# Optimization experiments

Measured on AMD Instinct MI355X. Metric: run time of the kernel, lower is better.

The kernel has to match this reference:

```python
import jax, jax.numpy as jnp
import numpy as np

B_GRAPHS, NODES, K, NGRID, C, BASIS = 8, 256, 16, 12, 128, 128
M = B_GRAPHS * NODES
TWO_PI = 2.0 * np.pi


def _knn_edges(pos):
    # within-graph kNN (includes self, like torch_cluster.knn(x, x, k))
    p = pos.reshape(B_GRAPHS, NODES, 3)
    d2 = jnp.sum((p[:, :, None, :] - p[:, None, :, :]) ** 2, axis=-1)  # [B,n,n]
    _, idx = jax.lax.top_k(-d2, K)                                     # [B,n,K]
    offs = jnp.arange(B_GRAPHS)[:, None, None] * NODES
    src = (idx + offs).reshape(-1)                                     # neighbor j (edge_index[0] after flip)
    tgt = jnp.broadcast_to(jnp.arange(NODES)[None, :, None] + offs, idx.shape).reshape(-1)
    return src, tgt


def _rff(x, B):
    proj = TWO_PI * (x @ B)
    return jnp.concatenate([jnp.cos(proj), jnp.sin(proj)], axis=-1)


def _basis_mlp(a, B, W1, b1, W2, b2):
    h = jax.nn.gelu(_rff(a, B) @ W1 + b1)
    return jax.nn.gelu(h @ W2 + b2)


def _layernorm(x, g, b):
    mu = jnp.mean(x, axis=-1, keepdims=True)
    var = jnp.var(x, axis=-1, keepdims=True)
    return (x - mu) * jax.lax.rsqrt(var + 1e-5) * g + b


def _interaction(x, kb_x, kb_R, src, tgt, Wkx, WkR, g, b, W1, b1, W2, b2, s):
    # spatial depthwise conv: gather -> per-edge kernel * x_j -> scatter-mean
    msg = (kb_x @ Wkx) * x[src]                                   # [E,NGRID,C]
    x1 = jax.ops.segment_sum(msg, tgt, num_segments=M) / K        # mean aggr (every node has exactly K in-edges)
    # fiber (orientation) depthwise conv
    kR = kb_R @ WkR                                               # [NGRID,NGRID,C]
    x2 = jnp.einsum('moc,poc->mpc', x1, kR) / NGRID
    # ConvNeXt-style pointwise MLP with layer scale + residual
    h = _layernorm(x2, g, b)
    h = jax.nn.gelu(h @ W1 + b1) @ W2 + b2
    return x + s * h


def _forward(x, pos_Rd, grid, Bx, BR, Wx1, bx1, Wx2, bx2, WR1, bR1, WR2, bR2,
             l1_Wkx, l1_WkR, l1_g, l1_b, l1_W1, l1_b1, l1_W2, l1_b2, l1_s,
             l2_Wkx, l2_WkR, l2_g, l2_b, l2_W1, l2_b1, l2_W2, l2_b2, l2_s):
    src, tgt = _knn_edges(pos_Rd)
    # equivariant edge attributes (edge_attr_r3s2_grid_mode)
    rel_pos_R = jnp.einsum('mi,ni->mn', grid, grid)[:, :, None]            # [NGRID,NGRID,1]
    rel_pos = pos_Rd[src] - pos_Rd[tgt]                                    # [E,3]
    rel_pos_z = jnp.einsum('ei,ni->en', rel_pos, grid)                     # [E,NGRID]
    rel_pos_xy = jnp.linalg.norm(rel_pos[:, None, :] - rel_pos_z[:, :, None] * grid[None, :, :], axis=-1)
    rel_pos_x = jnp.stack([rel_pos_xy, rel_pos_z], axis=-1)                # [E,NGRID,2]
    kb_x = _basis_mlp(rel_pos_x, Bx, Wx1, bx1, Wx2, bx2)                   # [E,NGRID,BASIS]
    kb_R = _basis_mlp(rel_pos_R, BR, WR1, bR1, WR2, bR2)                   # [NGRID,NGRID,BASIS]
    x = _interaction(x, kb_x, kb_R, src, tgt, l1_Wkx, l1_WkR, l1_g, l1_b, l1_W1, l1_b1, l1_W2, l1_b2, l1_s)
    x = _interaction(x, kb_x, kb_R, src, tgt, l2_Wkx, l2_WkR, l2_g, l2_b, l2_W1, l2_b1, l2_W2, l2_b2, l2_s)
    return x


def setup_inputs() -> dict:
    key = jax.random.key(0)
    ks = jax.random.split(key, 20)
    nrm = lambda k, shape, s: jax.random.normal(k, shape, jnp.float32) * s
    inp = {}
    inp['x'] = nrm(ks[0], (M, NGRID, C), 1.0)
    inp['pos_Rd'] = nrm(ks[1], (M, 3), 1.0)
    g = jax.random.normal(ks[2], (NGRID, 3), jnp.float32)
    inp['grid'] = g / jnp.linalg.norm(g, axis=-1, keepdims=True)           # unit S2 grid
    inp['Bx'] = nrm(ks[3], (2, C // 2), 10.0)                              # RFF, sigma=[10,10]
    inp['BR'] = nrm(ks[4], (1, C // 2), 10.0)                              # RFF, sigma=[10]
    inp['Wx1'] = nrm(ks[5], (C, C), C ** -0.5); inp['bx1'] = jnp.zeros((C,))
    inp['Wx2'] = nrm(ks[6], (C, BASIS), C ** -0.5); inp['bx2'] = jnp.zeros((BASIS,))
    inp['WR1'] = nrm(ks[7], (C, C), C ** -0.5); inp['bR1'] = jnp.zeros((C,))
    inp['WR2'] = nrm(ks[8], (C, BASIS), C ** -0.5); inp['bR2'] = jnp.zeros((BASIS,))
    i = 9
    for l in ('l1', 'l2'):
        inp[l + '_Wkx'] = nrm(ks[i], (BASIS, C), BASIS ** -0.5); i += 1
        inp[l + '_WkR'] = nrm(ks[i], (BASIS, C), BASIS ** -0.5); i += 1
        inp[l + '_g'] = jnp.ones((C,)); inp[l + '_b'] = jnp.zeros((C,))
        inp[l + '_W1'] = nrm(ks[i], (C, 4 * C), C ** -0.5); i += 1
        inp[l + '_b1'] = jnp.zeros((4 * C,))
        inp[l + '_W2'] = nrm(ks[i], (4 * C, C), (4 * C) ** -0.5); i += 1
        inp[l + '_b2'] = jnp.zeros((C,))
        inp[l + '_s'] = jnp.full((C,), 1e-2)
    return inp


def reference(x, pos_Rd, grid, Bx, BR, Wx1, bx1, Wx2, bx2, WR1, bR1, WR2, bR2,
              l1_Wkx, l1_WkR, l1_g, l1_b, l1_W1, l1_b1, l1_W2, l1_b2, l1_s,
              l2_Wkx, l2_WkR, l2_g, l2_b, l2_W1, l2_b1, l2_W2, l2_b2, l2_s):
    return _forward(x, pos_Rd, grid, Bx, BR, Wx1, bx1, Wx2, bx2, WR1, bR1, WR2, bR2,
                    l1_Wkx, l1_WkR, l1_g, l1_b, l1_W1, l1_b1, l1_W2, l1_b2, l1_s,
                    l2_Wkx, l2_WkR, l2_g, l2_b, l2_W1, l2_b1, l2_W2, l2_b2, l2_s)
```

## Files before the change

### kernel.cpp

```cpp
#include <hip/hip_runtime.h>
#include <hip/hip_bf16.h>
#include <math.h>

#define BG 8
#define NNODES 256
#define KNN 16
#define NG 12
#define CH 128
#define MTOT 2048
#define TWO_PI_F 6.283185307179586f

typedef __attribute__((ext_vector_type(8))) short bfrag;
typedef __attribute__((ext_vector_type(4))) float f32x4;


__device__ __forceinline__ float gelu_t(float x) {
  float x3 = x * x * x;
  float y = 0.7978845608028654f * (x + 0.044715f * x3);
  float e = __expf(2.0f * y);
  float th = 1.0f - 2.0f / (e + 1.0f);
  return 0.5f * x * (1.0f + th);
}

__device__ __forceinline__ unsigned packbf2(float a, float b) {
  unsigned ua = __float_as_uint(a), ub = __float_as_uint(b);
  ua = (ua + 0x7fffu + ((ua >> 16) & 1u)) >> 16;
  ub = (ub + 0x7fffu + ((ub >> 16) & 1u)) >> 16;
  return ua | (ub << 16);
}
__device__ __forceinline__ unsigned short f2bf(float f) {
  unsigned u = __float_as_uint(f);
  u = (u + 0x7fffu + ((u >> 16) & 1u)) >> 16;
  return (unsigned short)u;
}
__device__ __forceinline__ float ubf_lo(unsigned p) { return __uint_as_float(p << 16); }
__device__ __forceinline__ float ubf_hi(unsigned p) { return __uint_as_float(p & 0xffff0000u); }

__device__ __forceinline__ float gelu_s(float x) {
  const float A  = -2.0f * 0.7978845608028654f * 1.4426950408889634f;
  const float CA = A * 0.044715f;
  float x2 = x * x;
  float q  = __builtin_fmaf(CA, x2, A);
  float t  = x * q;
  float e; asm("v_exp_f32 %0, %1" : "=v"(e) : "v"(t));
  float d = 1.0f + e;
  float r; asm("v_rcp_f32 %0, %1" : "=v"(r) : "v"(d));
  return x * r;
}

__device__ __forceinline__ unsigned pkcvt(float a, float b) {
  unsigned r;
  asm("v_cvt_pk_bf16_f32 %0, %1, %2" : "=v"(r) : "v"(a), "v"(b));
  return r;
}

__device__ __forceinline__ void cossin(float w, float& c, float& s) {
  float f; asm("v_fract_f32 %0, %1" : "=v"(f) : "v"(w));
  asm("v_cos_f32 %0, %1" : "=v"(c) : "v"(f));
  asm("v_sin_f32 %0, %1" : "=v"(s) : "v"(f));
}

__device__ __forceinline__ unsigned long long shfl_xor64(unsigned long long v, int st) {
  unsigned lo = (unsigned)v, hi = (unsigned)(v >> 32);
  lo = __shfl_xor(lo, st, 64);
  hi = __shfl_xor(hi, st, 64);
  return ((unsigned long long)hi << 32) | lo;
}


__global__ __launch_bounds__(256) void knn_kernel(const float* __restrict__ pos,
                                                  int* __restrict__ knn) {
  __shared__ float sx[NNODES], sy[NNODES], sz[NNODES];
  int w = threadIdx.x >> 6, lane = threadIdx.x & 63;
  int node = blockIdx.x * 4 + w;
  int b = node >> 8;
  int gbase = b * NNODES;
  int t = threadIdx.x;
  sx[t] = pos[(gbase + t) * 3 + 0];
  sy[t] = pos[(gbase + t) * 3 + 1];
  sz[t] = pos[(gbase + t) * 3 + 2];
  __syncthreads();
  int i = node & 255;
  float xi = sx[i], yi = sy[i], zi = sz[i];
  unsigned long long key[4];
#pragma unroll
  for (int u = 0; u < 4; ++u) {
    int j = lane * 4 + u;
    float dx = xi - sx[j], dy = yi - sy[j], dz = zi - sz[j];
    float d = dx * dx + dy * dy + dz * dz;
    key[u] = ((unsigned long long)__float_as_uint(d) << 32) | (unsigned)j;
  }
  {
    unsigned long long tmp;
#define CSWAP(a, bq) if (key[bq] < key[a]) { tmp = key[a]; key[a] = key[bq]; key[bq] = tmp; }
    CSWAP(0, 1) CSWAP(2, 3) CSWAP(0, 2) CSWAP(1, 3) CSWAP(1, 2)
#undef CSWAP
  }
  int ptr = 0;
#pragma unroll 1
  for (int r = 0; r < KNN; ++r) {
    unsigned long long cand = (ptr < 4) ? key[ptr] : ~0ULL;
    unsigned long long mn = cand;
#pragma unroll
    for (int st = 1; st < 64; st <<= 1) {
      unsigned long long o = shfl_xor64(mn, st);
      if (o < mn) mn = o;
    }
    if (cand == mn) ptr++;
    if (lane == 0) knn[node * KNN + r] = gbase + (int)(mn & 0xffffffffu);
  }
}


__global__ void kbr_kernel(const float* __restrict__ grid, const float* __restrict__ BR,
                           const float* __restrict__ WR1, const float* __restrict__ bR1,
                           const float* __restrict__ WR2, const float* __restrict__ bR2,
                           const float* __restrict__ WkR1, const float* __restrict__ WkR2,
                           float* __restrict__ kR1, float* __restrict__ kR2) {
  int r = blockIdx.x;
  int p = r / NG, o = r % NG;
  int c = threadIdx.x;
  float a = grid[p * 3 + 0] * grid[o * 3 + 0] + grid[p * 3 + 1] * grid[o * 3 + 1] +
            grid[p * 3 + 2] * grid[o * 3 + 2];
  __shared__ float fb[CH], hh[CH];
  {
    int j = c & 63;
    float pv = TWO_PI_F * (a * BR[j]);
    fb[c] = (c < 64) ? cosf(pv) : sinf(pv);
  }
  __syncthreads();
  float acc = bR1[c];
  for (int i = 0; i < CH; ++i) acc += fb[i] * WR1[i * CH + c];
  float h1 = gelu_t(acc);
  __syncthreads();
  hh[c] = h1;
  __syncthreads();
  acc = bR2[c];
  for (int i = 0; i < CH; ++i) acc += hh[i] * WR2[i * CH + c];
  float h2 = gelu_t(acc);
  __syncthreads();
  fb[c] = h2;
  __syncthreads();
  float t1 = 0.f, t2 = 0.f;
  for (int i = 0; i < CH; ++i) {
    float v = fb[i];
    t1 += v * WkR1[i * CH + c];
    t2 += v * WkR2[i * CH + c];
  }
  kR1[r * CH + c] = t1;
  kR2[r * CH + c] = t2;
}


__global__ void einsum_kernel(const float* __restrict__ x1, const float* __restrict__ kR,
                              float* __restrict__ x2) {
  int m = blockIdx.x, c = threadIdx.x;
  float v[NG];
#pragma unroll
  for (int o = 0; o < NG; ++o) v[o] = x1[((size_t)m * NG + o) * CH + c];
#pragma unroll
  for (int p = 0; p < NG; ++p) {
    float acc = 0.f;
#pragma unroll
    for (int o = 0; o < NG; ++o) acc += v[o] * kR[(p * NG + o) * CH + c];
    x2[((size_t)m * NG + p) * CH + c] = acc * (1.0f / NG);
  }
}


__device__ __forceinline__ void pack_body(const float* __restrict__ W, int K, int N,
                                          unsigned short* __restrict__ out, int tid) {
  int lane = tid & 63;
  int t = tid >> 6;
  int ksteps = K / 32;
  int ks = t % ksteps, tile = t / ksteps;
  int col = tile * 16 + (lane & 15);
  int k0 = ks * 32 + (lane >> 4) * 8;
#pragma unroll
  for (int j = 0; j < 8; ++j)
    out[(size_t)tid * 8 + j] = f2bf(W[(size_t)(k0 + j) * N + col]);
}

__global__ __launch_bounds__(256) void pack_all_kernel(
    const float* __restrict__ W1a, const float* __restrict__ W2a,
    const float* __restrict__ W1b, const float* __restrict__ W2b,
    const float* __restrict__ wx1, const float* __restrict__ wx2,
    const float* __restrict__ wk1, const float* __restrict__ wk2,
    unsigned short* __restrict__ o1a, unsigned short* __restrict__ o2a,
    unsigned short* __restrict__ o1b, unsigned short* __restrict__ o2b,
    unsigned short* __restrict__ ox1, unsigned short* __restrict__ ox2,
    unsigned short* __restrict__ ok1, unsigned short* __restrict__ ok2) {
  int blk = blockIdx.x;
  if (blk < 32)        pack_body(W1a, CH, 4 * CH, o1a, blk * 256 + threadIdx.x);
  else if (blk < 64)   pack_body(W2a, 4 * CH, CH, o2a, (blk - 32) * 256 + threadIdx.x);
  else if (blk < 96)   pack_body(W1b, CH, 4 * CH, o1b, (blk - 64) * 256 + threadIdx.x);
  else if (blk < 128)  pack_body(W2b, 4 * CH, CH, o2b, (blk - 96) * 256 + threadIdx.x);
  else if (blk < 136)  pack_body(wx1, CH, CH, ox1, (blk - 128) * 256 + threadIdx.x);
  else if (blk < 144)  pack_body(wx2, CH, CH, ox2, (blk - 136) * 256 + threadIdx.x);
  else if (blk < 152)  pack_body(wk1, CH, CH, ok1, (blk - 144) * 256 + threadIdx.x);
  else                 pack_body(wk2, CH, CH, ok2, (blk - 152) * 256 + threadIdx.x);
}


__global__ __launch_bounds__(256) void kbx_fused_kernel(
    const float* __restrict__ pos, const int* __restrict__ knn,
    const float* __restrict__ grid, const float* __restrict__ Bx,
    const uint4* __restrict__ w1f, const float* __restrict__ bx1,
    const uint4* __restrict__ w2f, const float* __restrict__ bx2,
    const uint4* __restrict__ wk1f, const uint4* __restrict__ wk2f,
    const float* __restrict__ x, const float* __restrict__ kR,
    uint2* __restrict__ t2g, float* __restrict__ x2out) {
  __shared__ uint4 hb[4][3][256];
  float* x1s = (float*)hb;
  int m = blockIdx.x;
  int tid = threadIdx.x, lane = tid & 63, w = tid >> 6;
  int r = lane & 15, gq = lane >> 4;

  int src = knn[m * KNN + r];
  float rx = pos[src * 3 + 0] - pos[m * 3 + 0];
  float ry = pos[src * 3 + 1] - pos[m * 3 + 1];
  float rz = pos[src * 3 + 2] - pos[m * 3 + 2];

  float4 brA0 = *(const float4*)(Bx + gq * 8);
  float4 brA1 = *(const float4*)(Bx + gq * 8 + 4);
  float4 brB0 = *(const float4*)(Bx + 32 + gq * 8);
  float4 brB1 = *(const float4*)(Bx + 32 + gq * 8 + 4);
  float4 bzA0 = *(const float4*)(Bx + 64 + gq * 8);
  float4 bzA1 = *(const float4*)(Bx + 64 + gq * 8 + 4);
  float4 bzB0 = *(const float4*)(Bx + 96 + gq * 8);
  float4 bzB1 = *(const float4*)(Bx + 96 + gq * 8 + 4);
  float brA[8] = {brA0.x, brA0.y, brA0.z, brA0.w, brA1.x, brA1.y, brA1.z, brA1.w};
  float brB[8] = {brB0.x, brB0.y, brB0.z, brB0.w, brB1.x, brB1.y, brB1.z, brB1.w};
  float bzA[8] = {bzA0.x, bzA0.y, bzA0.z, bzA0.w, bzA1.x, bzA1.y, bzA1.z, bzA1.w};
  float bzB[8] = {bzB0.x, bzB0.y, bzB0.z, bzB0.w, bzB1.x, bzB1.y, bzB1.z, bzB1.w};

  bfrag ff[3][4];
#pragma unroll
  for (int t = 0; t < 3; ++t) {
    int o = w * 3 + t;
    float gx = grid[o * 3 + 0], gy = grid[o * 3 + 1], gz = grid[o * 3 + 2];
    float z = rx * gx + ry * gy + rz * gz;
    float ux = rx - z * gx, uy = ry - z * gy, uz = rz - z * gz;
    float rxy = sqrtf(ux * ux + uy * uy + uz * uz);
    float cA[8], sA[8], cB[8], sB[8];
#pragma unroll
    for (int u = 0; u < 8; ++u) {
      float wA = __builtin_fmaf(z, bzA[u], rxy * brA[u]);
      float wB = __builtin_fmaf(z, bzB[u], rxy * brB[u]);
      cossin(wA, cA[u], sA[u]);
      cossin(wB, cB[u], sB[u]);
    }
    uint4 q;
    q.x = pkcvt(cA[0], cA[1]); q.y = pkcvt(cA[2], cA[3]);
    q.z = pkcvt(cA[4], cA[5]); q.w = pkcvt(cA[6], cA[7]);
    ff[t][0] = __builtin_bit_cast(bfrag, q);
    q.x = pkcvt(cB[0], cB[1]); q.y = pkcvt(cB[2], cB[3]);
    q.z = pkcvt(cB[4], cB[5]); q.w = pkcvt(cB[6], cB[7]);
    ff[t][1] = __builtin_bit_cast(bfrag, q);
    q.x = pkcvt(sA[0], sA[1]); q.y = pkcvt(sA[2], sA[3]);
    q.z = pkcvt(sA[4], sA[5]); q.w = pkcvt(sA[6], sA[7]);
    ff[t][2] = __builtin_bit_cast(bfrag, q);
    q.x = pkcvt(sB[0], sB[1]); q.y = pkcvt(sB[2], sB[3]);
    q.z = pkcvt(sB[4], sB[5]); q.w = pkcvt(sB[6], sB[7]);
    ff[t][3] = __builtin_bit_cast(bfrag, q);
  }

#pragma unroll 1
  for (int jt = 0; jt < 8; ++jt) {
    bfrag wf[4];
#pragma unroll
    for (int ks = 0; ks < 4; ++ks)
      wf[ks] = __builtin_bit_cast(bfrag, w1f[(jt * 4 + ks) * 64 + lane]);
    float4 bb = *(const float4*)(bx1 + jt * 16 + gq * 4);
    int cu = jt * 2 + (gq >> 1);
#pragma unroll
    for (int t = 0; t < 3; ++t) {
      f32x4 acc;
      acc[0] = bb.x; acc[1] = bb.y; acc[2] = bb.z; acc[3] = bb.w;
#pragma unroll
      for (int ks = 0; ks < 4; ++ks)
        acc = __builtin_amdgcn_mfma_f32_16x16x32_bf16(wf[ks], ff[t][ks], acc, 0, 0, 0);
      unsigned p0 = pkcvt(gelu_s(acc[0]), gelu_s(acc[1]));
      unsigned p1 = pkcvt(gelu_s(acc[2]), gelu_s(acc[3]));
      ((uint2*)&hb[w][t][0])[r * 32 + ((cu ^ r) << 1) + (gq & 1)] = make_uint2(p0, p1);
    }
  }
  bfrag h1f[3][4];
#pragma unroll
  for (int t = 0; t < 3; ++t)
#pragma unroll
    for (int ks = 0; ks < 4; ++ks)
      h1f[t][ks] = __builtin_bit_cast(bfrag, hb[w][t][r * 16 + ((ks * 4 + gq) ^ r)]);

#pragma unroll 1
  for (int jt = 0; jt < 8; ++jt) {
    bfrag wf[4];
#pragma unroll
    for (int ks = 0; ks < 4; ++ks)
      wf[ks] = __builtin_bit_cast(bfrag, w2f[(jt * 4 + ks) * 64 + lane]);
    float4 bb = *(const float4*)(bx2 + jt * 16 + gq * 4);
    int cu = jt * 2 + (gq >> 1);
#pragma unroll
    for (int t = 0; t < 3; ++t) {
      f32x4 acc;
      acc[0] = bb.x; acc[1] = bb.y; acc[2] = bb.z; acc[3] = bb.w;
#pragma unroll
      for (int ks = 0; ks < 4; ++ks)
        acc = __builtin_amdgcn_mfma_f32_16x16x32_bf16(wf[ks], h1f[t][ks], acc, 0, 0, 0);
      unsigned p0 = pkcvt(gelu_s(acc[0]), gelu_s(acc[1]));
      unsigned p1 = pkcvt(gelu_s(acc[2]), gelu_s(acc[3]));
      ((uint2*)&hb[w][t][0])[r * 32 + ((cu ^ r) << 1) + (gq & 1)] = make_uint2(p0, p1);
    }
  }
  bfrag h2f[3][4];
#pragma unroll
  for (int t = 0; t < 3; ++t)
#pragma unroll
    for (int ks = 0; ks < 4; ++ks)
      h2f[t][ks] = __builtin_bit_cast(bfrag, hb[w][t][r * 16 + ((ks * 4 + gq) ^ r)]);

  __syncthreads();

#pragma unroll 1
  for (int jt = 0; jt < 8; ++jt) {
    bfrag wf[4];
#pragma unroll
    for (int ks = 0; ks < 4; ++ks)
      wf[ks] = __builtin_bit_cast(bfrag, wk1f[(jt * 4 + ks) * 64 + lane]);
#pragma unroll
    for (int t = 0; t < 3; ++t) {
      int o = w * 3 + t;
      f32x4 acc;
      acc[0] = 0.f; acc[1] = 0.f; acc[2] = 0.f; acc[3] = 0.f;
#pragma unroll
      for (int ks = 0; ks < 4; ++ks)
        acc = __builtin_amdgcn_mfma_f32_16x16x32_bf16(wf[ks], h2f[t][ks], acc, 0, 0, 0);
      float4 xv = *(const float4*)(x + ((size_t)src * NG + o) * CH + jt * 16 + gq * 4);
      acc[0] *= xv.x; acc[1] *= xv.y; acc[2] *= xv.z; acc[3] *= xv.w;
#pragma unroll
      for (int st = 1; st < 16; st <<= 1) {
        acc[0] += __shfl_xor(acc[0], st, 64);
        acc[1] += __shfl_xor(acc[1], st, 64);
        acc[2] += __shfl_xor(acc[2], st, 64);
        acc[3] += __shfl_xor(acc[3], st, 64);
      }
      if (r == 0) {
        int c0 = jt * 16 + gq * 4;
        float4 sv;
        sv.x = acc[0] * (1.f / 16.f); sv.y = acc[1] * (1.f / 16.f);
        sv.z = acc[2] * (1.f / 16.f); sv.w = acc[3] * (1.f / 16.f);
        *(float4*)&x1s[o * CH + c0] = sv;
      }
    }
  }

#pragma unroll 1
  for (int jt = 0; jt < 8; ++jt) {
    bfrag wf[4];
#pragma unroll
    for (int ks = 0; ks < 4; ++ks)
      wf[ks] = __builtin_bit_cast(bfrag, wk2f[(jt * 4 + ks) * 64 + lane]);
#pragma unroll
    for (int t = 0; t < 3; ++t) {
      int tile = m * NG + w * 3 + t;
      f32x4 acc;
      acc[0] = 0.f; acc[1] = 0.f; acc[2] = 0.f; acc[3] = 0.f;
#pragma unroll
      for (int ks = 0; ks < 4; ++ks)
        acc = __builtin_amdgcn_mfma_f32_16x16x32_bf16(wf[ks], h2f[t][ks], acc, 0, 0, 0);
      uint2 pv;
      pv.x = pkcvt(acc[0], acc[1]);
      pv.y = pkcvt(acc[2], acc[3]);
      t2g[((size_t)tile * 8 + jt) * 64 + lane] = pv;
    }
  }
  __syncthreads();

  int c = tid & 127, p0 = tid >> 7;
  float v[NG];
#pragma unroll
  for (int o = 0; o < NG; ++o) v[o] = x1s[o * CH + c];
#pragma unroll
  for (int pp = 0; pp < 6; ++pp) {
    int p = p0 * 6 + pp;
    float acc = 0.f;
#pragma unroll
    for (int o = 0; o < NG; ++o) acc += v[o] * kR[(p * NG + o) * CH + c];
    x2out[((size_t)m * NG + p) * CH + c] = acc * (1.0f / NG);
  }
}


__global__ __launch_bounds__(256) void msg3b_kernel(
    const float* __restrict__ x, const int* __restrict__ knn,
    const uint2* __restrict__ t2g, const float* __restrict__ kR,
    float* __restrict__ x2out) {
  __shared__ float x1s[NG][CH];
  int m = blockIdx.x;
  int tid = threadIdx.x, lane = tid & 63, w = tid >> 6;
  int r = lane & 15, gq = lane >> 4;
  int src = knn[m * KNN + r];

#pragma unroll 1
  for (int jt = 0; jt < 8; ++jt) {
#pragma unroll
    for (int t = 0; t < 3; ++t) {
      int o = w * 3 + t;
      int tile = m * NG + o;
      uint2 tv = t2g[((size_t)tile * 8 + jt) * 64 + lane];
      float4 xv = *(const float4*)(x + ((size_t)src * NG + o) * CH + jt * 16 + gq * 4);
      float a0 = ubf_lo(tv.x) * xv.x;
      float a1 = ubf_hi(tv.x) * xv.y;
      float a2 = ubf_lo(tv.y) * xv.z;
      float a3 = ubf_hi(tv.y) * xv.w;
#pragma unroll
      for (int st = 1; st < 16; st <<= 1) {
        a0 += __shfl_xor(a0, st, 64);
        a1 += __shfl_xor(a1, st, 64);
        a2 += __shfl_xor(a2, st, 64);
        a3 += __shfl_xor(a3, st, 64);
      }
      if (r == 0) {
        int c0 = jt * 16 + gq * 4;
        x1s[o][c0 + 0] = a0 * (1.f / 16.f);
        x1s[o][c0 + 1] = a1 * (1.f / 16.f);
        x1s[o][c0 + 2] = a2 * (1.f / 16.f);
        x1s[o][c0 + 3] = a3 * (1.f / 16.f);
      }
    }
  }
  __syncthreads();

  int c = tid & 127, p0 = tid >> 7;
  float v[NG];
#pragma unroll
  for (int o = 0; o < NG; ++o) v[o] = x1s[o][c];
#pragma unroll
  for (int pp = 0; pp < 6; ++pp) {
    int p = p0 * 6 + pp;
    float acc = 0.f;
#pragma unroll
    for (int o = 0; o < NG; ++o) acc += v[o] * kR[(p * NG + o) * CH + c];
    x2out[((size_t)m * NG + p) * CH + c] = acc * (1.0f / NG);
  }
}


__global__ __launch_bounds__(256) void msg_mfma_kernel(
    const float* __restrict__ x, const float* __restrict__ pos,
    const int* __restrict__ knn, const float* __restrict__ grid,
    const float* __restrict__ Bx,
    const uint4* __restrict__ w1f, const float* __restrict__ bx1,
    const uint4* __restrict__ w2f, const float* __restrict__ bx2,
    const uint4* __restrict__ wkf,
    float* __restrict__ x1out) {
  __shared__ uint4 hb[4][3][256];
  int m = blockIdx.x;
  int tid = threadIdx.x, lane = tid & 63, w = tid >> 6;
  int r = lane & 15, gq = lane >> 4;

  int src = knn[m * KNN + r];
  float rx = pos[src * 3 + 0] - pos[m * 3 + 0];
  float ry = pos[src * 3 + 1] - pos[m * 3 + 1];
  float rz = pos[src * 3 + 2] - pos[m * 3 + 2];

  bfrag ff[3][4];
#pragma unroll
  for (int t = 0; t < 3; ++t) {
    int o = w * 3 + t;
    float gx = grid[o * 3 + 0], gy = grid[o * 3 + 1], gz = grid[o * 3 + 2];
    float z = rx * gx + ry * gy + rz * gz;
    float ux = rx - z * gx, uy = ry - z * gy, uz = rz - z * gz;
    float rxy = sqrtf(ux * ux + uy * uy + uz * uz);
#pragma unroll
    for (int ks = 0; ks < 4; ++ks) {
      uint4 q;
      unsigned pk[4];
#pragma unroll
      for (int jh = 0; jh < 4; ++jh) {
        float v[2];
#pragma unroll
        for (int u = 0; u < 2; ++u) {
          int i = ks * 32 + gq * 8 + jh * 2 + u;
          int j = i & 63;
          float pv = TWO_PI_F * (rxy * Bx[j] + z * Bx[64 + j]);
          v[u] = (i < 64) ? __cosf(pv) : __sinf(pv);
        }
        pk[jh] = packbf2(v[0], v[1]);
      }
      q.x = pk[0]; q.y = pk[1]; q.z = pk[2]; q.w = pk[3];
      ff[t][ks] = __builtin_bit_cast(bfrag, q);
    }
  }

#pragma unroll 1
  for (int jt = 0; jt < 8; ++jt) {
    bfrag wf[4];
#pragma unroll
    for (int ks = 0; ks < 4; ++ks)
      wf[ks] = __builtin_bit_cast(bfrag, w1f[(jt * 4 + ks) * 64 + lane]);
    float4 bb = *(const float4*)(bx1 + jt * 16 + gq * 4);
    int cu = jt * 2 + (gq >> 1);
#pragma unroll
    for (int t = 0; t < 3; ++t) {
      f32x4 acc;
      acc[0] = bb.x; acc[1] = bb.y; acc[2] = bb.z; acc[3] = bb.w;
#pragma unroll
      for (int ks = 0; ks < 4; ++ks)
        acc = __builtin_amdgcn_mfma_f32_16x16x32_bf16(wf[ks], ff[t][ks], acc, 0, 0, 0);
      unsigned p0 = packbf2(gelu_t(acc[0]), gelu_t(acc[1]));
      unsigned p1 = packbf2(gelu_t(acc[2]), gelu_t(acc[3]));
      ((uint2*)&hb[w][t][0])[r * 32 + ((cu ^ r) << 1) + (gq & 1)] = make_uint2(p0, p1);
    }
  }
  bfrag h1f[3][4];
#pragma unroll
  for (int t = 0; t < 3; ++t)
#pragma unroll
    for (int ks = 0; ks < 4; ++ks)
      h1f[t][ks] = __builtin_bit_cast(bfrag, hb[w][t][r * 16 + ((ks * 4 + gq) ^ r)]);

#pragma unroll 1
  for (int jt = 0; jt < 8; ++jt) {
    bfrag wf[4];
#pragma unroll
    for (int ks = 0; ks < 4; ++ks)
      wf[ks] = __builtin_bit_cast(bfrag, w2f[(jt * 4 + ks) * 64 + lane]);
    float4 bb = *(const float4*)(bx2 + jt * 16 + gq * 4);
    int cu = jt * 2 + (gq >> 1);
#pragma unroll
    for (int t = 0; t < 3; ++t) {
      f32x4 acc;
      acc[0] = bb.x; acc[1] = bb.y; acc[2] = bb.z; acc[3] = bb.w;
#pragma unroll
      for (int ks = 0; ks < 4; ++ks)
        acc = __builtin_amdgcn_mfma_f32_16x16x32_bf16(wf[ks], h1f[t][ks], acc, 0, 0, 0);
      unsigned p0 = packbf2(gelu_t(acc[0]), gelu_t(acc[1]));
      unsigned p1 = packbf2(gelu_t(acc[2]), gelu_t(acc[3]));
      ((uint2*)&hb[w][t][0])[r * 32 + ((cu ^ r) << 1) + (gq & 1)] = make_uint2(p0, p1);
    }
  }
  bfrag h2f[3][4];
#pragma unroll
  for (int t = 0; t < 3; ++t)
#pragma unroll
    for (int ks = 0; ks < 4; ++ks)
      h2f[t][ks] = __builtin_bit_cast(bfrag, hb[w][t][r * 16 + ((ks * 4 + gq) ^ r)]);

#pragma unroll 1
  for (int jt = 0; jt < 8; ++jt) {
    bfrag wf[4];
#pragma unroll
    for (int ks = 0; ks < 4; ++ks)
      wf[ks] = __builtin_bit_cast(bfrag, wkf[(jt * 4 + ks) * 64 + lane]);
#pragma unroll
    for (int t = 0; t < 3; ++t) {
      int o = w * 3 + t;
      f32x4 acc;
      acc[0] = 0.f; acc[1] = 0.f; acc[2] = 0.f; acc[3] = 0.f;
#pragma unroll
      for (int ks = 0; ks < 4; ++ks)
        acc = __builtin_amdgcn_mfma_f32_16x16x32_bf16(wf[ks], h2f[t][ks], acc, 0, 0, 0);
      float4 xv = *(const float4*)(x + ((size_t)src * NG + o) * CH + jt * 16 + gq * 4);
      acc[0] *= xv.x; acc[1] *= xv.y; acc[2] *= xv.z; acc[3] *= xv.w;
#pragma unroll
      for (int st = 1; st < 16; st <<= 1) {
        acc[0] += __shfl_xor(acc[0], st, 64);
        acc[1] += __shfl_xor(acc[1], st, 64);
        acc[2] += __shfl_xor(acc[2], st, 64);
        acc[3] += __shfl_xor(acc[3], st, 64);
      }
      if (r == 0) {
        float4 sv;
        sv.x = acc[0] * (1.f / 16.f); sv.y = acc[1] * (1.f / 16.f);
        sv.z = acc[2] * (1.f / 16.f); sv.w = acc[3] * (1.f / 16.f);
        *(float4*)(x1out + ((size_t)m * NG + o) * CH + jt * 16 + gq * 4) = sv;
      }
    }
  }
}


__global__ __launch_bounds__(256) void mlp_mfma_kernel(
    const float* __restrict__ xin, const float* __restrict__ x2,
    const float* __restrict__ g, const float* __restrict__ b,
    const uint4* __restrict__ w1t, const float* __restrict__ b1,
    const uint4* __restrict__ w2t, const float* __restrict__ b2,
    const float* __restrict__ s, float* __restrict__ xout) {
  __shared__ uint4 smem[1280];
  int tid = threadIdx.x;
  int rowbase = blockIdx.x * 16;

  {
    int row = tid >> 4, p = tid & 15;
    const float4* xr = (const float4*)(x2 + (size_t)(rowbase + row) * CH + p * 8);
    float4 v0 = xr[0], v1 = xr[1];
    float sum = v0.x + v0.y + v0.z + v0.w + v1.x + v1.y + v1.z + v1.w;
    sum += __shfl_xor(sum, 1, 64); sum += __shfl_xor(sum, 2, 64);
    sum += __shfl_xor(sum, 4, 64); sum += __shfl_xor(sum, 8, 64);
    float mu = sum * (1.0f / CH);
    float sq = 0.f;
    {
      float d;
      d = v0.x - mu; sq += d * d; d = v0.y - mu; sq += d * d;
      d = v0.z - mu; sq += d * d; d = v0.w - mu; sq += d * d;
      d = v1.x - mu; sq += d * d; d = v1.y - mu; sq += d * d;
      d = v1.z - mu; sq += d * d; d = v1.w - mu; sq += d * d;
    }
    sq += __shfl_xor(sq, 1, 64); sq += __shfl_xor(sq, 2, 64);
    sq += __shfl_xor(sq, 4, 64); sq += __shfl_xor(sq, 8, 64);
    float rstd = rsqrtf(sq * (1.0f / CH) + 1e-5f);
    const float4* gv = (const float4*)(g + p * 8);
    const float4* bv = (const float4*)(b + p * 8);
    float4 g0 = gv[0], g1 = gv[1], b0 = bv[0], b1v = bv[1];
    float n0 = (v0.x - mu) * rstd * g0.x + b0.x;
    float n1 = (v0.y - mu) * rstd * g0.y + b0.y;
    float n2 = (v0.z - mu) * rstd * g0.z + b0.z;
    float n3 = (v0.w - mu) * rstd * g0.w + b0.w;
    float n4 = (v1.x - mu) * rstd * g1.x + b1v.x;
    float n5 = (v1.y - mu) * rstd * g1.y + b1v.y;
    float n6 = (v1.z - mu) * rstd * g1.z + b1v.z;
    float n7 = (v1.w - mu) * rstd * g1.w + b1v.w;
    uint4 pk;
    pk.x = packbf2(n0, n1); pk.y = packbf2(n2, n3);
    pk.z = packbf2(n4, n5); pk.w = packbf2(n6, n7);
    smem[row * 16 + (p ^ row)] = pk;
  }
  __syncthreads();

  int lane = tid & 63, w = tid >> 6;
  int r = lane & 15, gq = lane >> 4;

  bfrag xf[4];
#pragma unroll
  for (int ks = 0; ks < 4; ++ks) {
    uint4 raw = smem[r * 16 + ((ks * 4 + gq) ^ r)];
    xf[ks] = __builtin_bit_cast(bfrag, raw);
  }

  uint2* hb2 = (uint2*)smem;
#pragma unroll 1
  for (int jj = 0; jj < 8; ++jj) {
    int jt = w * 8 + jj;
    f32x4 acc;
    {
      float4 bb = *(const float4*)(b1 + jt * 16 + gq * 4);
      acc[0] = bb.x; acc[1] = bb.y; acc[2] = bb.z; acc[3] = bb.w;
    }
#pragma unroll
    for (int ks = 0; ks < 4; ++ks) {
      uint4 raw = w1t[(jt * 4 + ks) * 64 + lane];
      bfrag a = __builtin_bit_cast(bfrag, raw);
      acc = __builtin_amdgcn_mfma_f32_16x16x32_bf16(a, xf[ks], acc, 0, 0, 0);
    }
    unsigned p0 = packbf2(gelu_t(acc[0]), gelu_t(acc[1]));
    unsigned p1 = packbf2(gelu_t(acc[2]), gelu_t(acc[3]));
    int sl = (jt * 2 + (gq >> 1)) ^ r;
    hb2[512 + r * 128 + sl * 2 + (gq & 1)] = make_uint2(p0, p1);
  }
  __syncthreads();

#pragma unroll 1
  for (int cc = 0; cc < 2; ++cc) {
    int ct = w * 2 + cc;
    f32x4 acc;
    {
      float4 bb = *(const float4*)(b2 + ct * 16 + gq * 4);
      acc[0] = bb.x; acc[1] = bb.y; acc[2] = bb.z; acc[3] = bb.w;
    }
#pragma unroll
    for (int ks = 0; ks < 16; ++ks) {
      uint4 hraw = smem[256 + r * 64 + ((ks * 4 + gq) ^ r)];
      bfrag hf = __builtin_bit_cast(bfrag, hraw);
      uint4 wraw = w2t[(ct * 16 + ks) * 64 + lane];
      bfrag wf = __builtin_bit_cast(bfrag, wraw);
      acc = __builtin_amdgcn_mfma_f32_16x16x32_bf16(wf, hf, acc, 0, 0, 0);
    }
    int c0 = ct * 16 + gq * 4;
    size_t ro = (size_t)(rowbase + r) * CH + c0;
    float4 xi = *(const float4*)(xin + ro);
    float4 sv = *(const float4*)(s + c0);
    float4 ov;
    ov.x = xi.x + sv.x * acc[0];
    ov.y = xi.y + sv.y * acc[1];
    ov.z = xi.z + sv.z * acc[2];
    ov.w = xi.w + sv.w * acc[3];
    *(float4*)(xout + ro) = ov;
  }
}


extern "C" void kernel_launch(void* const* d_in, const int* in_sizes, int n_in,
                              void* d_out, int out_size, void* d_ws, size_t ws_size,
                              hipStream_t stream) {
  (void)in_sizes; (void)n_in; (void)out_size;
  const float* x    = (const float*)d_in[0];
  const float* pos  = (const float*)d_in[1];
  const float* grid = (const float*)d_in[2];
  const float* Bx   = (const float*)d_in[3];
  float* out = (float*)d_out;

  char* wsb = (char*)d_ws;
  int* knn   = (int*)wsb;
  float* kR1 = (float*)(wsb + 131072);
  float* kR2 = kR1 + NG * NG * CH;
  float* x1  = kR2 + NG * NG * CH;
  float* x2  = x1 + (size_t)MTOT * NG * CH;
  unsigned short* w1ta = (unsigned short*)(x2 + (size_t)MTOT * NG * CH);
  unsigned short* w2ta = w1ta + 65536;
  unsigned short* w1tb = w2ta + 65536;
  unsigned short* w2tb = w1tb + 65536;
  unsigned short* wx1f = w2tb + 65536;
  unsigned short* wx2f = wx1f + 16384;
  unsigned short* wk1f = wx2f + 16384;
  unsigned short* wk2f = wk1f + 16384;
  uint2* t2g = (uint2*)(wk2f + 16384);
  size_t need = (size_t)26099712 + (size_t)MTOT * NG * 4 * 64 * 16;
  bool big_ws = ws_size >= need;

  knn_kernel<<<MTOT / 4, 256, 0, stream>>>(pos, knn);
  kbr_kernel<<<NG * NG, CH, 0, stream>>>(grid, (const float*)d_in[4],
                                         (const float*)d_in[9], (const float*)d_in[10],
                                         (const float*)d_in[11], (const float*)d_in[12],
                                         (const float*)d_in[14], (const float*)d_in[23],
                                         kR1, kR2);
  pack_all_kernel<<<160, 256, 0, stream>>>(
      (const float*)d_in[17], (const float*)d_in[19],
      (const float*)d_in[26], (const float*)d_in[28],
      (const float*)d_in[5], (const float*)d_in[7],
      (const float*)d_in[13], (const float*)d_in[22],
      w1ta, w2ta, w1tb, w2tb, wx1f, wx2f, wk1f, wk2f);

  if (big_ws) {
    kbx_fused_kernel<<<MTOT, 256, 0, stream>>>(pos, knn, grid, Bx,
        (const uint4*)wx1f, (const float*)d_in[6],
        (const uint4*)wx2f, (const float*)d_in[8],
        (const uint4*)wk1f, (const uint4*)wk2f,
        x, kR1, t2g, x2);
    mlp_mfma_kernel<<<(MTOT * NG) / 16, 256, 0, stream>>>(x, x2,
        (const float*)d_in[15], (const float*)d_in[16],
        (const uint4*)w1ta, (const float*)d_in[18],
        (const uint4*)w2ta, (const float*)d_in[20],
        (const float*)d_in[21], out);
    msg3b_kernel<<<MTOT, 256, 0, stream>>>(out, knn, (const uint2*)t2g, kR2, x2);
    mlp_mfma_kernel<<<(MTOT * NG) / 16, 256, 0, stream>>>(out, x2,
        (const float*)d_in[24], (const float*)d_in[25],
        (const uint4*)w1tb, (const float*)d_in[27],
        (const uint4*)w2tb, (const float*)d_in[29],
        (const float*)d_in[30], out);
  } else {
    msg_mfma_kernel<<<MTOT, 256, 0, stream>>>(x, pos, knn, grid, Bx,
        (const uint4*)wx1f, (const float*)d_in[6],
        (const uint4*)wx2f, (const float*)d_in[8],
        (const uint4*)wk1f, x1);
    einsum_kernel<<<MTOT, CH, 0, stream>>>(x1, kR1, x2);
    mlp_mfma_kernel<<<(MTOT * NG) / 16, 256, 0, stream>>>(x, x2,
        (const float*)d_in[15], (const float*)d_in[16],
        (const uint4*)w1ta, (const float*)d_in[18],
        (const uint4*)w2ta, (const float*)d_in[20],
        (const float*)d_in[21], out);
    msg_mfma_kernel<<<MTOT, 256, 0, stream>>>(out, pos, knn, grid, Bx,
        (const uint4*)wx1f, (const float*)d_in[6],
        (const uint4*)wx2f, (const float*)d_in[8],
        (const uint4*)wk2f, x1);
    einsum_kernel<<<MTOT, CH, 0, stream>>>(x1, kR2, x2);
    mlp_mfma_kernel<<<(MTOT * NG) / 16, 256, 0, stream>>>(out, x2,
        (const float*)d_in[24], (const float*)d_in[25],
        (const uint4*)w1tb, (const float*)d_in[27],
        (const uint4*)w2tb, (const float*)d_in[29],
        (const float*)d_in[30], out);
  }
}
```

Measured before the change: 232.9 us.

## Stream hidden MLP tiles through smaller LDS buffer and raise occupancy bound

The two per-edge basis MLP layers now produce output in chunks of two column tiles, converting each chunk straight into the next layer's k-slice fragment instead of staging the whole hidden layer in LDS. This quarters the shared-memory scratch per block and allows a launch bound of 4 blocks per SM, aiming for higher occupancy. It adds a minimum-occupancy hint that may force register spills, given the large fragment arrays kept in registers.

```diff
diff --git a/kernel.cpp b/kernel.cpp
--- a/kernel.cpp
+++ b/kernel.cpp
@@ -202,7 +202,7 @@
 }
 
 
-__global__ __launch_bounds__(256) void kbx_fused_kernel(
+__global__ __launch_bounds__(256, 4) void kbx_fused_kernel(
     const float* __restrict__ pos, const int* __restrict__ knn,
     const float* __restrict__ grid, const float* __restrict__ Bx,
     const uint4* __restrict__ w1f, const float* __restrict__ bx1,
@@ -210,8 +210,8 @@
     const uint4* __restrict__ wk1f, const uint4* __restrict__ wk2f,
     const float* __restrict__ x, const float* __restrict__ kR,
     uint2* __restrict__ t2g, float* __restrict__ x2out) {
-  __shared__ uint4 hb[4][3][256];
-  float* x1s = (float*)hb;
+  __shared__ uint2 hbuf[4][3][128];
+  float* x1s = (float*)hbuf;
   int m = blockIdx.x;
   int tid = threadIdx.x, lane = tid & 63, w = tid >> 6;
   int r = lane & 15, gq = lane >> 4;
@@ -265,59 +265,63 @@
     ff[t][3] = __builtin_bit_cast(bfrag, q);
   }
 
-#pragma unroll 1
-  for (int jt = 0; jt < 8; ++jt) {
-    bfrag wf[4];
-#pragma unroll
-    for (int ks = 0; ks < 4; ++ks)
-      wf[ks] = __builtin_bit_cast(bfrag, w1f[(jt * 4 + ks) * 64 + lane]);
-    float4 bb = *(const float4*)(bx1 + jt * 16 + gq * 4);
-    int cu = jt * 2 + (gq >> 1);
-#pragma unroll
-    for (int t = 0; t < 3; ++t) {
-      f32x4 acc;
-      acc[0] = bb.x; acc[1] = bb.y; acc[2] = bb.z; acc[3] = bb.w;
-#pragma unroll
-      for (int ks = 0; ks < 4; ++ks)
-        acc = __builtin_amdgcn_mfma_f32_16x16x32_bf16(wf[ks], ff[t][ks], acc, 0, 0, 0);
-      unsigned p0 = pkcvt(gelu_s(acc[0]), gelu_s(acc[1]));
-      unsigned p1 = pkcvt(gelu_s(acc[2]), gelu_s(acc[3]));
-      ((uint2*)&hb[w][t][0])[r * 32 + ((cu ^ r) << 1) + (gq & 1)] = make_uint2(p0, p1);
-    }
-  }
   bfrag h1f[3][4];
-#pragma unroll
-  for (int t = 0; t < 3; ++t)
-#pragma unroll
-    for (int ks = 0; ks < 4; ++ks)
-      h1f[t][ks] = __builtin_bit_cast(bfrag, hb[w][t][r * 16 + ((ks * 4 + gq) ^ r)]);
-
-#pragma unroll 1
-  for (int jt = 0; jt < 8; ++jt) {
-    bfrag wf[4];
-#pragma unroll
-    for (int ks = 0; ks < 4; ++ks)
-      wf[ks] = __builtin_bit_cast(bfrag, w2f[(jt * 4 + ks) * 64 + lane]);
-    float4 bb = *(const float4*)(bx2 + jt * 16 + gq * 4);
-    int cu = jt * 2 + (gq >> 1);
-#pragma unroll
-    for (int t = 0; t < 3; ++t) {
-      f32x4 acc;
-      acc[0] = bb.x; acc[1] = bb.y; acc[2] = bb.z; acc[3] = bb.w;
-#pragma unroll
-      for (int ks = 0; ks < 4; ++ks)
-        acc = __builtin_amdgcn_mfma_f32_16x16x32_bf16(wf[ks], h1f[t][ks], acc, 0, 0, 0);
-      unsigned p0 = pkcvt(gelu_s(acc[0]), gelu_s(acc[1]));
-      unsigned p1 = pkcvt(gelu_s(acc[2]), gelu_s(acc[3]));
-      ((uint2*)&hb[w][t][0])[r * 32 + ((cu ^ r) << 1) + (gq & 1)] = make_uint2(p0, p1);
-    }
-  }
+#pragma unroll 1
+  for (int ks = 0; ks < 4; ++ks) {
+#pragma unroll
+    for (int jq = 0; jq < 2; ++jq) {
+      int jt = ks * 2 + jq;
+      bfrag wf[4];
+#pragma unroll
+      for (int kk = 0; kk < 4; ++kk)
+        wf[kk] = __builtin_bit_cast(bfrag, w1f[(jt * 4 + kk) * 64 + lane]);
+      float4 bb = *(const float4*)(bx1 + jt * 16 + gq * 4);
+#pragma unroll
+      for (int t = 0; t < 3; ++t) {
+        f32x4 acc;
+        acc[0] = bb.x; acc[1] = bb.y; acc[2] = bb.z; acc[3] = bb.w;
+#pragma unroll
+        for (int kk = 0; kk < 4; ++kk)
+          acc = __builtin_amdgcn_mfma_f32_16x16x32_bf16(wf[kk], ff[t][kk], acc, 0, 0, 0);
+        unsigned p0 = pkcvt(gelu_s(acc[0]), gelu_s(acc[1]));
+        unsigned p1 = pkcvt(gelu_s(acc[2]), gelu_s(acc[3]));
+        hbuf[w][t][jq * 64 + r * 4 + gq] = make_uint2(p0, p1);
+      }
+    }
+#pragma unroll
+    for (int t = 0; t < 3; ++t)
+      h1f[t][ks] = __builtin_bit_cast(bfrag,
+          ((const uint4*)&hbuf[w][t][0])[(gq >> 1) * 32 + r * 2 + (gq & 1)]);
+  }
+
   bfrag h2f[3][4];
-#pragma unroll
-  for (int t = 0; t < 3; ++t)
-#pragma unroll
-    for (int ks = 0; ks < 4; ++ks)
-      h2f[t][ks] = __builtin_bit_cast(bfrag, hb[w][t][r * 16 + ((ks * 4 + gq) ^ r)]);
+#pragma unroll 1
+  for (int ks = 0; ks < 4; ++ks) {
+#pragma unroll
+    for (int jq = 0; jq < 2; ++jq) {
+      int jt = ks * 2 + jq;
+      bfrag wf[4];
+#pragma unroll
+      for (int kk = 0; kk < 4; ++kk)
+        wf[kk] = __builtin_bit_cast(bfrag, w2f[(jt * 4 + kk) * 64 + lane]);
+      float4 bb = *(const float4*)(bx2 + jt * 16 + gq * 4);
+#pragma unroll
+      for (int t = 0; t < 3; ++t) {
+        f32x4 acc;
+        acc[0] = bb.x; acc[1] = bb.y; acc[2] = bb.z; acc[3] = bb.w;
+#pragma unroll
+        for (int kk = 0; kk < 4; ++kk)
+          acc = __builtin_amdgcn_mfma_f32_16x16x32_bf16(wf[kk], h1f[t][kk], acc, 0, 0, 0);
+        unsigned p0 = pkcvt(gelu_s(acc[0]), gelu_s(acc[1]));
+        unsigned p1 = pkcvt(gelu_s(acc[2]), gelu_s(acc[3]));
+        hbuf[w][t][jq * 64 + r * 4 + gq] = make_uint2(p0, p1);
+      }
+    }
+#pragma unroll
+    for (int t = 0; t < 3; ++t)
+      h2f[t][ks] = __builtin_bit_cast(bfrag,
+          ((const uint4*)&hbuf[w][t][0])[(gq >> 1) * 32 + r * 2 + (gq & 1)]);
+  }
 
   __syncthreads();
 
```

New measurement: 263.9 us. 1.13x slower.
